# Kernel optimization log

Measured on AMD Instinct MI355X. Metric: run time of the kernel, lower is better.

Reference implementation:

```python
import jax, jax.numpy as jnp
import numpy as np

E = 131072
IN_F = 64
OUT_F = 64
BOND_TYPE = 10  # num_type=4 -> 4*5/2
INIT_VAL = 0.01


def setup_inputs() -> dict:
    key = jax.random.key(0)
    k1, k2, k3, k4 = jax.random.split(key, 4)
    batch_ij = jax.random.randint(k1, (E,), 0, BOND_TYPE)
    batch_descriptor = jax.random.normal(k2, (E, IN_F, 1), dtype=jnp.float32)
    layer1 = INIT_VAL * jax.random.normal(k3, (BOND_TYPE, OUT_F, IN_F), dtype=jnp.float32)
    lin_w = INIT_VAL * jax.random.normal(k4, (OUT_F, IN_F), dtype=jnp.float32)
    lin_b = jnp.zeros((OUT_F,), dtype=jnp.float32)
    return {
        "batch_ij": batch_ij,
        "batch_descriptor": batch_descriptor,
        "layer1": layer1,
        "lin_w": lin_w,
        "lin_b": lin_b,
    }


def reference(batch_ij, batch_descriptor, layer1, lin_w, lin_b):
    # gather per-edge weight matrix by bond type, then batched matmul
    desc = batch_descriptor[..., 0]                       # [E, in]
    W_e = layer1[batch_ij]                                # [E, out, in] (large gather)
    out = jnp.einsum("eoi,ei->eo", W_e, desc)            # bmm
    out = jnp.tanh(out)                                   # ACT
    adjust = desc @ lin_w.T + lin_b                        # linear_adjust
    return (out + adjust)[..., None]                       # [E, out, 1]
```

## Files before the change

### kernel.cpp

```cpp
#include <hip/hip_runtime.h>
#include <hip/hip_bf16.h>

typedef __attribute__((ext_vector_type(8))) short bf16x8;
typedef __attribute__((ext_vector_type(4))) float f32x4;

#define NBLK 256

__device__ __forceinline__ unsigned short f2bf(float f) {
    unsigned u = __float_as_uint(f);
    return (unsigned short)((u + 0x7fffu + ((u >> 16) & 1u)) >> 16);
}

__device__ __forceinline__ bf16x8 pack8(float4 x, float4 y) {
    bf16x8 r;
    r[0] = (short)f2bf(x.x); r[1] = (short)f2bf(x.y);
    r[2] = (short)f2bf(x.z); r[3] = (short)f2bf(x.w);
    r[4] = (short)f2bf(y.x); r[5] = (short)f2bf(y.y);
    r[6] = (short)f2bf(y.z); r[7] = (short)f2bf(y.w);
    return r;
}

__device__ __forceinline__ float ftanh(float x) {
    float e = __expf(2.f * x);
    return 1.f - 2.f / (e + 1.f);
}

__global__ __launch_bounds__(512, 2) void k_fused(
    const int* __restrict__ ij, const float* __restrict__ desc,
    const float* __restrict__ layer1, const float* __restrict__ lin_w,
    const float* __restrict__ lin_b, float* __restrict__ out, int E) {

    __shared__ __align__(16) short wsm[11 * 512 * 8];

    for (int idx = threadIdx.x; idx < 11 * 512; idx += 512) {
        const int m = idx >> 9;
        const int fl = idx & 511;
        const int fi = fl >> 6, l = fl & 63;
        const int nt = fi >> 1, kk = fi & 1;
        const float* src = (m < 10) ? (layer1 + m * 4096) : lin_w;
        const float* sp = src + (nt * 16 + (l & 15)) * 64 + kk * 32 + (l >> 4) * 8;
        float4 x = *(const float4*)sp;
        float4 y = *(const float4*)(sp + 4);
        *(bf16x8*)(&wsm[idx * 8]) = pack8(x, y);
    }

    const int lane = threadIdx.x & 63;
    const int col = lane & 15;
    const int g = lane >> 4;
    const int kb = g * 8;
    const bf16x8 zero8 = {0, 0, 0, 0, 0, 0, 0, 0};

    __syncthreads();

    bf16x8 al[4][2];
    #pragma unroll
    for (int fi = 0; fi < 8; ++fi)
        al[fi >> 1][fi & 1] = *(const bf16x8*)(&wsm[((80 + fi) * 64 + lane) * 8]);

    const int gw = blockIdx.x * 8 + (threadIdx.x >> 6);
    const int base = gw * 64;
    if (base >= E) return;

    const int e_own = min(base + lane, E - 1);
    const int ty_own = ij[e_own];
    int rank = 0, below = 0;
    #pragma unroll
    for (int t = 0; t < 10; ++t) {
        const unsigned long long m = __ballot(ty_own == t);
        if (ty_own == t) rank = below + (int)__popcll(m & ((1ull << lane) - 1ull));
        below += (int)__popcll(m);
    }
    const int e_sorted = __builtin_amdgcn_ds_permute(rank << 2, e_own);
    const int ty_sorted = __builtin_amdgcn_ds_permute(rank << 2, ty_own);

    #pragma unroll 1
    for (int tp = 0; tp < 4; ++tp) {
        const int pbase = tp * 16;
        const int e_t = __shfl(e_sorted, pbase + col);
        const int ty_t = __shfl(ty_sorted, pbase + col);
        const int ty_lo = __shfl(ty_sorted, pbase);
        const int ty_hi = __shfl(ty_sorted, pbase + 15);

        const float* dp = desc + (size_t)e_t * 64 + kb;
        const float4 x0 = *(const float4*)dp,        y0 = *(const float4*)(dp + 4);
        const float4 x1 = *(const float4*)(dp + 32), y1 = *(const float4*)(dp + 36);
        const bf16x8 b0 = pack8(x0, y0);
        const bf16x8 b1 = pack8(x1, y1);

        f32x4 zL[4], zW[4];
        #pragma unroll
        for (int nt = 0; nt < 4; ++nt) {
            f32x4 z = {0.f, 0.f, 0.f, 0.f};
            z = __builtin_amdgcn_mfma_f32_16x16x32_bf16(al[nt][0], b0, z, 0, 0, 0);
            zL[nt] = __builtin_amdgcn_mfma_f32_16x16x32_bf16(al[nt][1], b1, z, 0, 0, 0);
            zW[nt] = (f32x4){0.f, 0.f, 0.f, 0.f};
        }

        #pragma unroll 1
        for (int m = ty_lo; m <= ty_hi; ++m) {
            if (!__any(ty_t == m)) continue;
            const bf16x8 m0 = (ty_t == m) ? b0 : zero8;
            const bf16x8 m1 = (ty_t == m) ? b1 : zero8;
            #pragma unroll
            for (int nt = 0; nt < 4; ++nt) {
                const bf16x8 f0 = *(const bf16x8*)(&wsm[((m * 8 + nt * 2 + 0) * 64 + lane) * 8]);
                const bf16x8 f1 = *(const bf16x8*)(&wsm[((m * 8 + nt * 2 + 1) * 64 + lane) * 8]);
                zW[nt] = __builtin_amdgcn_mfma_f32_16x16x32_bf16(f0, m0, zW[nt], 0, 0, 0);
                zW[nt] = __builtin_amdgcn_mfma_f32_16x16x32_bf16(f1, m1, zW[nt], 0, 0, 0);
            }
        }

        float* op = out + (size_t)e_t * 64 + g * 4;
        #pragma unroll
        for (int nt = 0; nt < 4; ++nt) {
            const float4 bias = *(const float4*)(lin_b + nt * 16 + g * 4);
            f32x4 r;
            r[0] = ftanh(zW[nt][0]) + zL[nt][0] + bias.x;
            r[1] = ftanh(zW[nt][1]) + zL[nt][1] + bias.y;
            r[2] = ftanh(zW[nt][2]) + zL[nt][2] + bias.z;
            r[3] = ftanh(zW[nt][3]) + zL[nt][3] + bias.w;
            *(f32x4*)(op + nt * 16) = r;
        }
    }
}

extern "C" void kernel_launch(void* const* d_in, const int* in_sizes, int n_in,
                              void* d_out, int out_size, void* d_ws, size_t ws_size,
                              hipStream_t stream) {
    const int* ij = (const int*)d_in[0];
    const float* desc = (const float*)d_in[1];
    const float* layer1 = (const float*)d_in[2];
    const float* lin_w = (const float*)d_in[3];
    const float* lin_b = (const float*)d_in[4];
    float* out = (float*)d_out;
    const int E = in_sizes[0];

    k_fused<<<NBLK, 512, 0, stream>>>(ij, desc, layer1, lin_w, lin_b, out, E);
}
```

Measured before the change: 24.19 us.

## Prefetch descriptors and type sort before weight staging, software-pipeline tile loads

Moves the per-wave type ranking, the shuffle of sorted edge indices and the first descriptor tile load ahead of the shared-memory weight conversion and barrier. Global-load latency for the indices and first tile can then overlap the weight staging. Inside the tile loop, the next tile's descriptor rows are loaded before the current tile's MFMAs, giving double buffering. Bias loads are hoisted out of the loop. The cost is higher register pressure from the held arrays and the prefetch buffers, under a 512-thread, 2-block launch bound.

```diff
diff --git a/kernel.cpp b/kernel.cpp
--- a/kernel.cpp
+++ b/kernel.cpp
@@ -32,6 +32,45 @@
 
     __shared__ __align__(16) short wsm[11 * 512 * 8];
 
+    const int lane = threadIdx.x & 63;
+    const int col = lane & 15;
+    const int g = lane >> 4;
+    const int kb = g * 8;
+    const bf16x8 zero8 = {0, 0, 0, 0, 0, 0, 0, 0};
+
+    const int gw = blockIdx.x * 8 + (threadIdx.x >> 6);
+    const int base = gw * 64;
+    const bool active = base < E;
+
+    int e_arr[4], ty_arr[4], lo[4], hi[4];
+    float4 cx0, cy0, cx1, cy1;
+    if (active) {
+        const int e_own = min(base + lane, E - 1);
+        const int ty_own = ij[e_own];
+        int rank = 0, below = 0;
+        #pragma unroll
+        for (int t = 0; t < 10; ++t) {
+            const unsigned long long m = __ballot(ty_own == t);
+            if (ty_own == t) rank = below + (int)__popcll(m & ((1ull << lane) - 1ull));
+            below += (int)__popcll(m);
+        }
+        const int e_sorted = __builtin_amdgcn_ds_permute(rank << 2, e_own);
+        const int ty_sorted = __builtin_amdgcn_ds_permute(rank << 2, ty_own);
+        #pragma unroll
+        for (int tp = 0; tp < 4; ++tp) {
+            e_arr[tp] = __shfl(e_sorted, tp * 16 + col);
+            ty_arr[tp] = __shfl(ty_sorted, tp * 16 + col);
+            lo[tp] = __shfl(ty_sorted, tp * 16);
+            hi[tp] = __shfl(ty_sorted, tp * 16 + 15);
+        }
+        const float* dp = desc + (size_t)e_arr[0] * 64 + kb;
+        cx0 = *(const float4*)dp;        cy0 = *(const float4*)(dp + 4);
+        cx1 = *(const float4*)(dp + 32); cy1 = *(const float4*)(dp + 36);
+    }
+    float4 bias[4];
+    #pragma unroll
+    for (int nt = 0; nt < 4; ++nt) bias[nt] = *(const float4*)(lin_b + nt * 16 + g * 4);
+
     for (int idx = threadIdx.x; idx < 11 * 512; idx += 512) {
         const int m = idx >> 9;
         const int fl = idx & 511;
@@ -43,49 +82,26 @@
         float4 y = *(const float4*)(sp + 4);
         *(bf16x8*)(&wsm[idx * 8]) = pack8(x, y);
     }
+    __syncthreads();
 
-    const int lane = threadIdx.x & 63;
-    const int col = lane & 15;
-    const int g = lane >> 4;
-    const int kb = g * 8;
-    const bf16x8 zero8 = {0, 0, 0, 0, 0, 0, 0, 0};
-
-    __syncthreads();
+    if (!active) return;
 
     bf16x8 al[4][2];
     #pragma unroll
     for (int fi = 0; fi < 8; ++fi)
         al[fi >> 1][fi & 1] = *(const bf16x8*)(&wsm[((80 + fi) * 64 + lane) * 8]);
 
-    const int gw = blockIdx.x * 8 + (threadIdx.x >> 6);
-    const int base = gw * 64;
-    if (base >= E) return;
-
-    const int e_own = min(base + lane, E - 1);
-    const int ty_own = ij[e_own];
-    int rank = 0, below = 0;
-    #pragma unroll
-    for (int t = 0; t < 10; ++t) {
-        const unsigned long long m = __ballot(ty_own == t);
-        if (ty_own == t) rank = below + (int)__popcll(m & ((1ull << lane) - 1ull));
-        below += (int)__popcll(m);
-    }
-    const int e_sorted = __builtin_amdgcn_ds_permute(rank << 2, e_own);
-    const int ty_sorted = __builtin_amdgcn_ds_permute(rank << 2, ty_own);
-
     #pragma unroll 1
     for (int tp = 0; tp < 4; ++tp) {
-        const int pbase = tp * 16;
-        const int e_t = __shfl(e_sorted, pbase + col);
-        const int ty_t = __shfl(ty_sorted, pbase + col);
-        const int ty_lo = __shfl(ty_sorted, pbase);
-        const int ty_hi = __shfl(ty_sorted, pbase + 15);
-
-        const float* dp = desc + (size_t)e_t * 64 + kb;
-        const float4 x0 = *(const float4*)dp,        y0 = *(const float4*)(dp + 4);
-        const float4 x1 = *(const float4*)(dp + 32), y1 = *(const float4*)(dp + 36);
-        const bf16x8 b0 = pack8(x0, y0);
-        const bf16x8 b1 = pack8(x1, y1);
+        float4 nx0, ny0, nx1, ny1;
+        if (tp < 3) {
+            const float* np = desc + (size_t)e_arr[tp + 1] * 64 + kb;
+            nx0 = *(const float4*)np;        ny0 = *(const float4*)(np + 4);
+            nx1 = *(const float4*)(np + 32); ny1 = *(const float4*)(np + 36);
+        }
+        const bf16x8 b0 = pack8(cx0, cy0);
+        const bf16x8 b1 = pack8(cx1, cy1);
+        const int ty_t = ty_arr[tp];
 
         f32x4 zL[4], zW[4];
         #pragma unroll
@@ -97,7 +113,7 @@
         }
 
         #pragma unroll 1
-        for (int m = ty_lo; m <= ty_hi; ++m) {
+        for (int m = lo[tp]; m <= hi[tp]; ++m) {
             if (!__any(ty_t == m)) continue;
             const bf16x8 m0 = (ty_t == m) ? b0 : zero8;
             const bf16x8 m1 = (ty_t == m) ? b1 : zero8;
@@ -110,17 +126,18 @@
             }
         }
 
-        float* op = out + (size_t)e_t * 64 + g * 4;
+        float* op = out + (size_t)e_arr[tp] * 64 + g * 4;
         #pragma unroll
         for (int nt = 0; nt < 4; ++nt) {
-            const float4 bias = *(const float4*)(lin_b + nt * 16 + g * 4);
             f32x4 r;
-            r[0] = ftanh(zW[nt][0]) + zL[nt][0] + bias.x;
-            r[1] = ftanh(zW[nt][1]) + zL[nt][1] + bias.y;
-            r[2] = ftanh(zW[nt][2]) + zL[nt][2] + bias.z;
-            r[3] = ftanh(zW[nt][3]) + zL[nt][3] + bias.w;
+            r[0] = ftanh(zW[nt][0]) + zL[nt][0] + bias[nt].x;
+            r[1] = ftanh(zW[nt][1]) + zL[nt][1] + bias[nt].y;
+            r[2] = ftanh(zW[nt][2]) + zL[nt][2] + bias[nt].z;
+            r[3] = ftanh(zW[nt][3]) + zL[nt][3] + bias[nt].w;
             *(f32x4*)(op + nt * 16) = r;
         }
+
+        cx0 = nx0; cy0 = ny0; cx1 = nx1; cy1 = ny1;
     }
 }
 
```

After: 24.31 us. No clear change (+0.5%).

## Prepack bf16 weights in separate kernel and load to LDS asynchronously

Applied to the files above, without the earlier changes.

Weight conversion to bf16 fragment layout moves into a small pre-kernel that writes to workspace. The main kernel then copies the packed weights into LDS with direct global-to-LDS loads, overlapping them with the type-sort and descriptor prefetch. Blocks grow to 1024 threads with each wave pair splitting a 64-edge window, so every wave handles two 16-edge tiles instead of four. This adds a second kernel launch plus a fallback naive kernel for when the workspace is too small, and doubles the number of waves that each load the full weight set into LDS.

```diff
diff --git a/kernel.cpp b/kernel.cpp
--- a/kernel.cpp
+++ b/kernel.cpp
@@ -25,67 +25,97 @@
     return 1.f - 2.f / (e + 1.f);
 }
 
-__global__ __launch_bounds__(512, 2) void k_fused(
-    const int* __restrict__ ij, const float* __restrict__ desc,
-    const float* __restrict__ layer1, const float* __restrict__ lin_w,
-    const float* __restrict__ lin_b, float* __restrict__ out, int E) {
-
-    __shared__ __align__(16) short wsm[11 * 512 * 8];
-
-    for (int idx = threadIdx.x; idx < 11 * 512; idx += 512) {
-        const int m = idx >> 9;
-        const int fl = idx & 511;
-        const int fi = fl >> 6, l = fl & 63;
+__global__ void k_pack(const float* __restrict__ layer1, const float* __restrict__ lin_w,
+                       __hip_bfloat16* __restrict__ wpk) {
+    const int m = blockIdx.x;
+    const float* src = (m < 10) ? (layer1 + m * 4096) : lin_w;
+    __hip_bfloat16* dst = wpk + m * 4096;
+    for (int idx = threadIdx.x; idx < 512; idx += 256) {
+        const int fi = idx >> 6, l = idx & 63;
         const int nt = fi >> 1, kk = fi & 1;
-        const float* src = (m < 10) ? (layer1 + m * 4096) : lin_w;
         const float* sp = src + (nt * 16 + (l & 15)) * 64 + kk * 32 + (l >> 4) * 8;
         float4 x = *(const float4*)sp;
         float4 y = *(const float4*)(sp + 4);
-        *(bf16x8*)(&wsm[idx * 8]) = pack8(x, y);
-    }
-
-    const int lane = threadIdx.x & 63;
+        *(bf16x8*)(dst + idx * 8) = pack8(x, y);
+    }
+}
+
+__global__ __launch_bounds__(1024, 4) void k_main(
+    const int* __restrict__ ij, const float* __restrict__ desc,
+    const __hip_bfloat16* __restrict__ wpk, const float* __restrict__ lin_b,
+    float* __restrict__ out, int E) {
+
+    __shared__ __align__(16) short wsm[12 * 4096];
+
+    const int tid = threadIdx.x;
+    const int lane = tid & 63;
+    const int wid = tid >> 6;
     const int col = lane & 15;
     const int g = lane >> 4;
     const int kb = g * 8;
     const bf16x8 zero8 = {0, 0, 0, 0, 0, 0, 0, 0};
 
+    const int gwave = blockIdx.x * 16 + wid;
+    const int win = gwave >> 1;
+    const int base = win * 64;
+    const bool active = base < E;
+
+    int ty_own = 0, e_own = 0;
+    if (active) {
+        e_own = min(base + lane, E - 1);
+        ty_own = ij[e_own];
+    }
+
+    #pragma unroll
+    for (int it = 0; it < 6; ++it) {
+        const int off = it * 16384 + tid * 16;
+        __builtin_amdgcn_global_load_lds((const char*)wpk + off, (char*)wsm + off, 16, 0, 0);
+    }
+
+    int e_sorted = 0, ty_sorted = 0;
+    if (active) {
+        int rank = 0, below = 0;
+        #pragma unroll
+        for (int t = 0; t < 10; ++t) {
+            const unsigned long long m = __ballot(ty_own == t);
+            if (ty_own == t) rank = below + (int)__popcll(m & ((1ull << lane) - 1ull));
+            below += (int)__popcll(m);
+        }
+        e_sorted = __builtin_amdgcn_ds_permute(rank << 2, e_own);
+        ty_sorted = __builtin_amdgcn_ds_permute(rank << 2, ty_own);
+    }
+
+    const int tp0 = (wid & 1) * 2;
+    int e_t[2], ty_t[2], lo[2], hi[2];
+    float4 dx0[2], dy0[2], dx1[2], dy1[2];
+    if (active) {
+        #pragma unroll
+        for (int q = 0; q < 2; ++q) {
+            const int pb = (tp0 + q) * 16;
+            e_t[q] = __shfl(e_sorted, pb + col);
+            ty_t[q] = __shfl(ty_sorted, pb + col);
+            lo[q] = __shfl(ty_sorted, pb);
+            hi[q] = __shfl(ty_sorted, pb + 15);
+            const float* dp = desc + (size_t)e_t[q] * 64 + kb;
+            dx0[q] = *(const float4*)dp;        dy0[q] = *(const float4*)(dp + 4);
+            dx1[q] = *(const float4*)(dp + 32); dy1[q] = *(const float4*)(dp + 36);
+        }
+    }
+
     __syncthreads();
+
+    if (!active) return;
 
     bf16x8 al[4][2];
     #pragma unroll
     for (int fi = 0; fi < 8; ++fi)
         al[fi >> 1][fi & 1] = *(const bf16x8*)(&wsm[((80 + fi) * 64 + lane) * 8]);
 
-    const int gw = blockIdx.x * 8 + (threadIdx.x >> 6);
-    const int base = gw * 64;
-    if (base >= E) return;
-
-    const int e_own = min(base + lane, E - 1);
-    const int ty_own = ij[e_own];
-    int rank = 0, below = 0;
-    #pragma unroll
-    for (int t = 0; t < 10; ++t) {
-        const unsigned long long m = __ballot(ty_own == t);
-        if (ty_own == t) rank = below + (int)__popcll(m & ((1ull << lane) - 1ull));
-        below += (int)__popcll(m);
-    }
-    const int e_sorted = __builtin_amdgcn_ds_permute(rank << 2, e_own);
-    const int ty_sorted = __builtin_amdgcn_ds_permute(rank << 2, ty_own);
-
     #pragma unroll 1
-    for (int tp = 0; tp < 4; ++tp) {
-        const int pbase = tp * 16;
-        const int e_t = __shfl(e_sorted, pbase + col);
-        const int ty_t = __shfl(ty_sorted, pbase + col);
-        const int ty_lo = __shfl(ty_sorted, pbase);
-        const int ty_hi = __shfl(ty_sorted, pbase + 15);
-
-        const float* dp = desc + (size_t)e_t * 64 + kb;
-        const float4 x0 = *(const float4*)dp,        y0 = *(const float4*)(dp + 4);
-        const float4 x1 = *(const float4*)(dp + 32), y1 = *(const float4*)(dp + 36);
-        const bf16x8 b0 = pack8(x0, y0);
-        const bf16x8 b1 = pack8(x1, y1);
+    for (int q = 0; q < 2; ++q) {
+        const bf16x8 b0 = pack8(dx0[q], dy0[q]);
+        const bf16x8 b1 = pack8(dx1[q], dy1[q]);
+        const int tyq = ty_t[q];
 
         f32x4 zL[4], zW[4];
         #pragma unroll
@@ -97,10 +127,10 @@
         }
 
         #pragma unroll 1
-        for (int m = ty_lo; m <= ty_hi; ++m) {
-            if (!__any(ty_t == m)) continue;
-            const bf16x8 m0 = (ty_t == m) ? b0 : zero8;
-            const bf16x8 m1 = (ty_t == m) ? b1 : zero8;
+        for (int m = lo[q]; m <= hi[q]; ++m) {
+            if (!__any(tyq == m)) continue;
+            const bf16x8 m0 = (tyq == m) ? b0 : zero8;
+            const bf16x8 m1 = (tyq == m) ? b1 : zero8;
             #pragma unroll
             for (int nt = 0; nt < 4; ++nt) {
                 const bf16x8 f0 = *(const bf16x8*)(&wsm[((m * 8 + nt * 2 + 0) * 64 + lane) * 8]);
@@ -110,7 +140,7 @@
             }
         }
 
-        float* op = out + (size_t)e_t * 64 + g * 4;
+        float* op = out + (size_t)e_t[q] * 64 + g * 4;
         #pragma unroll
         for (int nt = 0; nt < 4; ++nt) {
             const float4 bias = *(const float4*)(lin_b + nt * 16 + g * 4);
@@ -121,6 +151,31 @@
             r[3] = ftanh(zW[nt][3]) + zL[nt][3] + bias.w;
             *(f32x4*)(op + nt * 16) = r;
         }
+    }
+}
+
+__global__ void k_naive(const int* __restrict__ ij, const float* __restrict__ desc,
+                        const float* __restrict__ layer1, const float* __restrict__ lin_w,
+                        const float* __restrict__ lin_b, float* __restrict__ out, int E) {
+    const int wid = (blockIdx.x * blockDim.x + threadIdx.x) >> 6;
+    const int lane = threadIdx.x & 63;
+    const int nw = (gridDim.x * blockDim.x) >> 6;
+    for (int e = wid; e < E; e += nw) {
+        const int t = ij[e];
+        const float d = desc[(size_t)e * 64 + lane];
+        const float* Wr = layer1 + t * 4096 + lane * 64;
+        const float* Lr = lin_w + lane * 64;
+        float a1 = 0.f, a2 = 0.f;
+        #pragma unroll
+        for (int i = 0; i < 64; i += 4) {
+            float4 w4 = *(const float4*)(Wr + i);
+            float4 l4 = *(const float4*)(Lr + i);
+            const float d0 = __shfl(d, i), d1 = __shfl(d, i + 1);
+            const float d2 = __shfl(d, i + 2), d3 = __shfl(d, i + 3);
+            a1 = fmaf(w4.x, d0, fmaf(w4.y, d1, fmaf(w4.z, d2, fmaf(w4.w, d3, a1))));
+            a2 = fmaf(l4.x, d0, fmaf(l4.y, d1, fmaf(l4.z, d2, fmaf(l4.w, d3, a2))));
+        }
+        out[(size_t)e * 64 + lane] = tanhf(a1) + a2 + lin_b[lane];
     }
 }
 
@@ -135,5 +190,13 @@
     float* out = (float*)d_out;
     const int E = in_sizes[0];
 
-    k_fused<<<NBLK, 512, 0, stream>>>(ij, desc, layer1, lin_w, lin_b, out, E);
-}
+    const size_t need = (size_t)12 * 4096 * sizeof(__hip_bfloat16) + 64;
+    if (ws_size < need) {
+        k_naive<<<2048, 256, 0, stream>>>(ij, desc, layer1, lin_w, lin_b, out, E);
+        return;
+    }
+    __hip_bfloat16* wpk = (__hip_bfloat16*)d_ws;
+
+    k_pack<<<11, 256, 0, stream>>>(layer1, lin_w, wpk);
+    k_main<<<NBLK, 1024, 0, stream>>>(ij, desc, wpk, lin_b, out, E);
+}
```

New measurement: 40.58 us. 1.68x slower.
